# Kernel optimization log

Hardware: AMD Instinct MI355X
Metric: run time of the kernel (lower is better)

## Reference

```python
import jax, jax.numpy as jnp
import numpy as np

B, S, E, H = 4, 2048, 1024, 128  # batch, seq_len, n_embeddings, head_size


def setup_inputs() -> dict:
    key = jax.random.key(0)
    kx, kq, kk, kv = jax.random.split(key, 4)
    x = jax.random.normal(kx, (B, S, E), dtype=jnp.float32)
    # nn.Linear(E, H, bias=False) weights, stored transposed so proj = x @ W
    Wq = jax.random.normal(kq, (E, H), dtype=jnp.float32) * 0.02
    Wk = jax.random.normal(kk, (E, H), dtype=jnp.float32) * 0.02
    Wv = jax.random.normal(kv, (E, H), dtype=jnp.float32) * 0.02
    return {"x": x, "Wq": Wq, "Wk": Wk, "Wv": Wv}


def reference(x, Wq, Wk, Wv):
    # Single causal self-attention head (dropout = identity, eval mode).
    q = jnp.einsum("bse,eh->bsh", x, Wq)  # [B,S,H]
    k = jnp.einsum("bse,eh->bsh", x, Wk)
    v = jnp.einsum("bse,eh->bsh", x, Wv)
    scale = 1.0 / jnp.sqrt(jnp.asarray(H, dtype=x.dtype))
    scores = jnp.einsum("bqh,bkh->bqk", q, k) * scale  # [B,S,S]
    causal = jnp.tril(jnp.ones((S, S), dtype=bool))
    scores = jnp.where(causal, scores, jnp.asarray(-jnp.inf, dtype=scores.dtype))
    weights = jax.nn.softmax(scores, axis=-1)
    out = jnp.einsum("bqk,bkh->bqh", weights, v)  # [B,S,H]
    return out
```

## Files before the change

### kernel.cpp

```cpp
#include <hip/hip_runtime.h>
#include <math.h>

#define BB 4
#define SS 2048
#define EE 1024
#define HH 128
#define PLANE (BB * SS * HH)
#define BPLANE (SS * HH)
#define AUNITS 144

typedef __bf16 bf16x8 __attribute__((ext_vector_type(8)));
typedef __bf16 bf16x4 __attribute__((ext_vector_type(4)));
typedef float f32x4 __attribute__((ext_vector_type(4)));

#define QSCALE (0.08838834764831845f * 1.4426950408889634f)

__global__ __launch_bounds__(256) void prep_w(
    const float* __restrict__ Wq, const float* __restrict__ Wk,
    const float* __restrict__ Wv, __bf16* __restrict__ WT) {
  __shared__ float LT[32 * 33];
  const int p = blockIdx.x >> 7;
  const int r = blockIdx.x & 127;
  const int kb = (r >> 2) * 32, nb = (r & 3) * 32;
  const float* __restrict__ W = (p == 0) ? Wq : (p == 1) ? Wk : Wv;
  const int t = threadIdx.x;
  const int kr = t >> 3, nc4 = (t & 7) * 4;
  const float4 v = *(const float4*)&W[(size_t)(kb + kr) * HH + nb + nc4];
  LT[(nc4 + 0) * 33 + kr] = v.x;
  LT[(nc4 + 1) * 33 + kr] = v.y;
  LT[(nc4 + 2) * 33 + kr] = v.z;
  LT[(nc4 + 3) * 33 + kr] = v.w;
  __syncthreads();
  const int n = t >> 3, kc = (t & 7) * 4;
  bf16x4 o;
#pragma unroll
  for (int i = 0; i < 4; ++i) o[i] = (__bf16)LT[n * 33 + kc + i];
  *(bf16x4*)&WT[(size_t)p * (HH * EE) + (size_t)(nb + n) * EE + kb + kc] = o;
}

__global__ __launch_bounds__(512, 2) void qkv_proj(
    const float* __restrict__ x, const __bf16* __restrict__ WT,
    __bf16* __restrict__ qkv) {
  __shared__ __align__(16) char smem[81920];
  __bf16* xs = (__bf16*)smem;
  __bf16* wsd = (__bf16*)(smem + 40960);

  const int t = threadIdx.x, w = t >> 6, lane = t & 63;
  const int quad = lane >> 4, l16 = lane & 15;
  const int kg = w >> 2, wl = w & 3;
  const int t2 = t & 255;
  const int mb = blockIdx.x * 128;
  const int proj = blockIdx.y;
  const __bf16* __restrict__ WTp = WT + (size_t)proj * (HH * EE);
  const int wm = (wl >> 1) * 64, wn = (wl & 1) * 64;
  const int kb0 = kg * 512;

  f32x4 acc[4][4];
#pragma unroll
  for (int i = 0; i < 4; ++i)
#pragma unroll
    for (int j = 0; j < 4; ++j) acc[i][j] = (f32x4){0.f, 0.f, 0.f, 0.f};

  {
    __bf16* xb = xs + (size_t)(kg * 2) * 5120;
    __bf16* wb = wsd + (size_t)(kg * 2) * 5120;
#pragma unroll
    for (int i = 0; i < 4; ++i) {
      const int idx = t2 + i * 256;
      const int row = idx >> 3, kc = (idx & 7) * 4;
      const float4 v = *(const float4*)&x[(size_t)(mb + row) * EE + kb0 + kc];
      bf16x4 bv;
      bv[0] = (__bf16)v.x; bv[1] = (__bf16)v.y;
      bv[2] = (__bf16)v.z; bv[3] = (__bf16)v.w;
      *(bf16x4*)&xb[row * 40 + kc] = bv;
    }
#pragma unroll
    for (int i = 0; i < 2; ++i) {
      const int idx = t2 + i * 256;
      const int n = idx >> 2, kc8 = (idx & 3) * 8;
      *(bf16x8*)&wb[n * 40 + kc8] =
          *(const bf16x8*)&WTp[(size_t)n * EE + kb0 + kc8];
    }
  }
  __syncthreads();

  for (int kt = 0; kt < 16; ++kt) {
    const int cur = kt & 1;
    float4 xr[4];
    bf16x8 wr[2];
    if (kt < 15) {
      const int kb = kb0 + (kt + 1) * 32;
#pragma unroll
      for (int i = 0; i < 4; ++i) {
        const int idx = t2 + i * 256;
        const int row = idx >> 3, kc = (idx & 7) * 4;
        xr[i] = *(const float4*)&x[(size_t)(mb + row) * EE + kb + kc];
      }
#pragma unroll
      for (int i = 0; i < 2; ++i) {
        const int idx = t2 + i * 256;
        const int n = idx >> 2, kc8 = (idx & 3) * 8;
        wr[i] = *(const bf16x8*)&WTp[(size_t)n * EE + kb + kc8];
      }
    }

    const __bf16* xb = xs + (size_t)(kg * 2 + cur) * 5120;
    const __bf16* wb = wsd + (size_t)(kg * 2 + cur) * 5120;
    bf16x8 af[4], bfr[4];
#pragma unroll
    for (int i = 0; i < 4; ++i)
      af[i] = *(const bf16x8*)&xb[(wm + i * 16 + l16) * 40 + quad * 8];
#pragma unroll
    for (int j = 0; j < 4; ++j)
      bfr[j] = *(const bf16x8*)&wb[(wn + j * 16 + l16) * 40 + quad * 8];
#pragma unroll
    for (int i = 0; i < 4; ++i)
#pragma unroll
      for (int j = 0; j < 4; ++j)
        acc[i][j] = __builtin_amdgcn_mfma_f32_16x16x32_bf16(
            af[i], bfr[j], acc[i][j], 0, 0, 0);

    if (kt < 15) {
      __bf16* xb1 = xs + (size_t)(kg * 2 + (cur ^ 1)) * 5120;
      __bf16* wb1 = wsd + (size_t)(kg * 2 + (cur ^ 1)) * 5120;
#pragma unroll
      for (int i = 0; i < 4; ++i) {
        const int idx = t2 + i * 256;
        const int row = idx >> 3, kc = (idx & 7) * 4;
        bf16x4 bv;
        bv[0] = (__bf16)xr[i].x; bv[1] = (__bf16)xr[i].y;
        bv[2] = (__bf16)xr[i].z; bv[3] = (__bf16)xr[i].w;
        *(bf16x4*)&xb1[row * 40 + kc] = bv;
      }
#pragma unroll
      for (int i = 0; i < 2; ++i) {
        const int idx = t2 + i * 256;
        const int n = idx >> 2, kc8 = (idx & 3) * 8;
        *(bf16x8*)&wb1[n * 40 + kc8] = wr[i];
      }
    }
    __syncthreads();
  }

  float* mbuf = (float*)smem;
  if (kg == 1) {
    float* mb = mbuf + (size_t)wl * 4096;
#pragma unroll
    for (int i = 0; i < 4; ++i)
#pragma unroll
      for (int j = 0; j < 4; ++j)
#pragma unroll
        for (int rr = 0; rr < 4; ++rr)
          mb[(i * 16 + quad * 4 + rr) * 64 + j * 16 + l16] = acc[i][j][rr];
  }
  __syncthreads();
  if (kg == 0) {
    const float* mb = mbuf + (size_t)wl * 4096;
#pragma unroll
    for (int i = 0; i < 4; ++i)
#pragma unroll
      for (int j = 0; j < 4; ++j)
#pragma unroll
        for (int rr = 0; rr < 4; ++rr)
          acc[i][j][rr] += mb[(i * 16 + quad * 4 + rr) * 64 + j * 16 + l16];

    if (proj < 2) {
      const float scale = (proj == 0) ? QSCALE : 1.0f;
      __bf16* outp = qkv + (size_t)proj * PLANE;
#pragma unroll
      for (int i = 0; i < 4; ++i) {
        const int s0 = mb == 0 ? 0 : 0;
        const int srow = (blockIdx.x * 128) + wm + i * 16 + quad * 4;
#pragma unroll
        for (int j = 0; j < 4; ++j)
#pragma unroll
          for (int rr = 0; rr < 4; ++rr)
            outp[(size_t)(srow + rr) * HH + wn + j * 16 + l16] =
                (__bf16)(acc[i][j][rr] * scale);
      }
    } else {
      __bf16* vtp = qkv + 2 * (size_t)PLANE;
#pragma unroll
      for (int i = 0; i < 4; ++i) {
        const int srow = (blockIdx.x * 128) + wm + i * 16 + quad * 4;
        const int bb = srow >> 11, sl = srow & 2047;
#pragma unroll
        for (int j = 0; j < 4; ++j) {
          const int d = wn + j * 16 + l16;
          bf16x4 vv;
#pragma unroll
          for (int rr = 0; rr < 4; ++rr) vv[rr] = (__bf16)acc[i][j][rr];
          *(bf16x4*)&vtp[(size_t)bb * BPLANE + (size_t)d * SS + sl] = vv;
        }
      }
    }
  }
}

__global__ __launch_bounds__(256, 2) void flash_attn_mfma(
    const __bf16* __restrict__ qkv, float* __restrict__ out,
    __bf16* __restrict__ Opart, float* __restrict__ lpart) {
  __shared__ __align__(16) __bf16 K_s[2][64 * 136];
  __shared__ __align__(16) __bf16 VT_s[2][128 * 72];

  const int t = threadIdx.x, w = t >> 6, lane = t & 63;
  const int quad = lane >> 4, l16 = lane & 15;
  const int b = blockIdx.x & 3;
  const int r = (AUNITS - 1) - (blockIdx.x >> 2);
  int g = 0;
  while (2 * (g + 1) * (g + 2) <= r) ++g;
  const int rem = r - 2 * g * (g + 1);
  const int nc = g + 1;
  const int tloc = rem / nc, c = rem % nc;
  const int tile = 4 * g + tloc;
  const int qrb = tile * 64;
  const int k0 = c * 256;
  const int kend = min(k0 + 256, qrb + 64);
  const int ntiles = (kend - k0) >> 6;
  const int qsb = qrb + w * 16;

  const size_t bq = (size_t)b * BPLANE;
  const __bf16* __restrict__ qp = qkv + bq;
  const __bf16* __restrict__ kp = qkv + PLANE + bq;
  const __bf16* __restrict__ vt = qkv + 2 * (size_t)PLANE + bq;

  bf16x8 qf[4];
#pragma unroll
  for (int cc = 0; cc < 4; ++cc)
    qf[cc] = *(const bf16x8*)&qp[(size_t)(qsb + l16) * HH + cc * 32 + quad * 8];

  f32x4 of[8];
#pragma unroll
  for (int f = 0; f < 8; ++f) of[f] = (f32x4){0.f, 0.f, 0.f, 0.f};
  float lp = 0.f;

  {
#pragma unroll
    for (int i = 0; i < 4; ++i) {
      const int idx = t + i * 256;
      const int row = idx >> 4, dc = (idx & 15) * 8;
      const int lam = (row & 32) + ((row & 4) ? 16 : 0) +
                      (((row & 31) >> 3) << 2) + (row & 3);
      *(bf16x8*)&K_s[0][lam * 136 + dc] =
          *(const bf16x8*)&kp[(size_t)(k0 + row) * HH + dc];
    }
#pragma unroll
    for (int i = 0; i < 4; ++i) {
      const int idx = t + i * 256;
      const int d = idx >> 3, kc = (idx & 7) * 8;
      *(bf16x8*)&VT_s[0][d * 72 + kc] =
          *(const bf16x8*)&vt[(size_t)d * SS + k0 + kc];
    }
  }
  __syncthreads();

  for (int jt = 0; jt < ntiles; ++jt) {
    const int cur = jt & 1;
    bf16x8 krg[4], vrg[4];
    if (jt + 1 < ntiles) {
      const int kb2 = k0 + (jt + 1) * 64;
#pragma unroll
      for (int i = 0; i < 4; ++i) {
        const int idx = t + i * 256;
        const int row = idx >> 4, dc = (idx & 15) * 8;
        krg[i] = *(const bf16x8*)&kp[(size_t)(kb2 + row) * HH + dc];
      }
#pragma unroll
      for (int i = 0; i < 4; ++i) {
        const int idx = t + i * 256;
        const int d = idx >> 3, kc = (idx & 7) * 8;
        vrg[i] = *(const bf16x8*)&vt[(size_t)d * SS + kb2 + kc];
      }
    }

    const __bf16* Kc = K_s[cur];
    const __bf16* Vc = VT_s[cur];
#pragma unroll
    for (int s32 = 0; s32 < 2; ++s32) {
      const int kabs = k0 + jt * 64 + s32 * 32;
      if (kabs <= qsb + 15) {
        bf16x8 ku[4], kv[4];
#pragma unroll
        for (int cc = 0; cc < 4; ++cc) {
          ku[cc] = *(const bf16x8*)&Kc[(s32 * 32 + l16) * 136 + cc * 32 + quad * 8];
          kv[cc] = *(const bf16x8*)&Kc[(s32 * 32 + 16 + l16) * 136 + cc * 32 + quad * 8];
        }
        f32x4 su = (f32x4){0.f, 0.f, 0.f, 0.f};
        f32x4 sv = (f32x4){0.f, 0.f, 0.f, 0.f};
#pragma unroll
        for (int cc = 0; cc < 4; ++cc) {
          su = __builtin_amdgcn_mfma_f32_16x16x32_bf16(ku[cc], qf[cc], su, 0, 0, 0);
          sv = __builtin_amdgcn_mfma_f32_16x16x32_bf16(kv[cc], qf[cc], sv, 0, 0, 0);
        }
        const int qg = qsb + l16;
        bf16x8 pa;
#pragma unroll
        for (int rr = 0; rr < 4; ++rr) {
          const int kU = kabs + quad * 8 + rr;
          const float eU = (kU <= qg) ? exp2f(su[rr]) : 0.f;
          const float eV = (kU + 4 <= qg) ? exp2f(sv[rr]) : 0.f;
          pa[rr] = (__bf16)eU;
          pa[4 + rr] = (__bf16)eV;
          lp += eU + eV;
        }
#pragma unroll
        for (int f = 0; f < 8; ++f) {
          const bf16x8 vb =
              *(const bf16x8*)&Vc[(f * 16 + l16) * 72 + s32 * 32 + quad * 8];
          of[f] = __builtin_amdgcn_mfma_f32_16x16x32_bf16(pa, vb, of[f], 0, 0, 0);
        }
      }
    }

    if (jt + 1 < ntiles) {
      const int nxt = cur ^ 1;
#pragma unroll
      for (int i = 0; i < 4; ++i) {
        const int idx = t + i * 256;
        const int row = idx >> 4, dc = (idx & 15) * 8;
        const int lam = (row & 32) + ((row & 4) ? 16 : 0) +
                        (((row & 31) >> 3) << 2) + (row & 3);
        *(bf16x8*)&K_s[nxt][lam * 136 + dc] = krg[i];
      }
#pragma unroll
      for (int i = 0; i < 4; ++i) {
        const int idx = t + i * 256;
        const int d = idx >> 3, kc = (idx & 7) * 8;
        *(bf16x8*)&VT_s[nxt][d * 72 + kc] = vrg[i];
      }
    }
    __syncthreads();
  }

  lp += __shfl_xor(lp, 16);
  lp += __shfl_xor(lp, 32);

  if (nc == 1) {
#pragma unroll
    for (int rr = 0; rr < 4; ++rr) {
      const float lrow = __shfl(lp, quad * 4 + rr);
      const float inv = 1.0f / lrow;
#pragma unroll
      for (int f = 0; f < 8; ++f)
        out[bq + (size_t)(qsb + quad * 4 + rr) * HH + f * 16 + l16] =
            of[f][rr] * inv;
    }
  } else {
    const int u = b * AUNITS + r;
    __bf16* op = Opart + (size_t)u * 8192;
#pragma unroll
    for (int f = 0; f < 8; ++f)
#pragma unroll
      for (int rr = 0; rr < 4; ++rr)
        op[(w * 16 + quad * 4 + rr) * 128 + f * 16 + l16] = (__bf16)of[f][rr];
    if (quad == 0) lpart[u * 64 + w * 16 + l16] = lp;
  }
}

__global__ __launch_bounds__(256) void attn_merge(
    const __bf16* __restrict__ Opart, const float* __restrict__ lpart,
    float* __restrict__ out) {
  const int b = blockIdx.x / 28;
  const int tile = 4 + (blockIdx.x % 28);
  const int g = tile >> 2, nc = g + 1, tloc = tile - 4 * g;
  const int u0 = b * AUNITS + 2 * g * (g + 1) + tloc * nc;
  const int t = threadIdx.x;
#pragma unroll
  for (int i = 0; i < 4; ++i) {
    const int idx = t + i * 256;
    const int e0 = idx * 8;
    const int row = e0 >> 7;
    float acc[8] = {0.f, 0.f, 0.f, 0.f, 0.f, 0.f, 0.f, 0.f};
    float lsum = 0.f;
    for (int cc = 0; cc < nc; ++cc) {
      const bf16x8 pv = *(const bf16x8*)&Opart[(size_t)(u0 + cc) * 8192 + e0];
#pragma unroll
      for (int k = 0; k < 8; ++k) acc[k] += (float)pv[k];
      lsum += lpart[(u0 + cc) * 64 + row];
    }
    const float inv = 1.0f / lsum;
    float4 r0, r1;
    r0.x = acc[0] * inv; r0.y = acc[1] * inv; r0.z = acc[2] * inv; r0.w = acc[3] * inv;
    r1.x = acc[4] * inv; r1.y = acc[5] * inv; r1.z = acc[6] * inv; r1.w = acc[7] * inv;
    float* op = out + (size_t)b * BPLANE + (size_t)tile * 8192 + e0;
    ((float4*)op)[0] = r0;
    ((float4*)op)[1] = r1;
  }
}

extern "C" void kernel_launch(void* const* d_in, const int* in_sizes, int n_in,
                              void* d_out, int out_size, void* d_ws, size_t ws_size,
                              hipStream_t stream) {
  const float* x  = (const float*)d_in[0];
  const float* Wq = (const float*)d_in[1];
  const float* Wk = (const float*)d_in[2];
  const float* Wv = (const float*)d_in[3];
  float* out = (float*)d_out;

  char* wsb = (char*)d_ws;
  __bf16* qkv = (__bf16*)wsb;
  __bf16* WT = (__bf16*)(wsb + (size_t)3 * PLANE * 2);
  __bf16* Opart = (__bf16*)(wsb + (size_t)3 * PLANE * 2 + (size_t)3 * HH * EE * 2);
  float* lpart = (float*)(wsb + (size_t)3 * PLANE * 2 + (size_t)3 * HH * EE * 2 +
                          (size_t)BB * AUNITS * 8192 * 2);

  prep_w<<<384, 256, 0, stream>>>(Wq, Wk, Wv, WT);
  qkv_proj<<<dim3(64, 3), 512, 0, stream>>>(x, WT, qkv);
  flash_attn_mfma<<<BB * AUNITS, 256, 0, stream>>>(qkv, out, Opart, lpart);
  attn_merge<<<BB * 28, 256, 0, stream>>>(Opart, lpart, out);
}
```

Baseline: 129.6 us.

## Shrink projection tiles, split attention into finer KV chunks, single-buffer LDS

The QKV projection moves from 128-row, split-K 512-thread blocks to 32-row 256-thread blocks with no split-K reduction, launching many more blocks. Attention work units are re-partitioned into 128-key chunks (272 units per batch instead of 144) with a new triangular index mapping, and the merge kernel is adjusted to match. The flash kernel drops LDS double buffering in favour of register prefetch plus two barriers per tile, cutting shared memory so three blocks fit per CU. The aim is better load balance and occupancy across CUs. The cost is more partial outputs to merge, more barriers, and more reloading of the projection weight tiles.

```diff
diff --git a/kernel.cpp b/kernel.cpp
--- a/kernel.cpp
+++ b/kernel.cpp
@@ -7,7 +7,7 @@
 #define HH 128
 #define PLANE (BB * SS * HH)
 #define BPLANE (SS * HH)
-#define AUNITS 144
+#define AUNITS 272
 
 typedef __bf16 bf16x8 __attribute__((ext_vector_type(8)));
 typedef __bf16 bf16x4 __attribute__((ext_vector_type(4)));
@@ -38,184 +38,130 @@
   *(bf16x4*)&WT[(size_t)p * (HH * EE) + (size_t)(nb + n) * EE + kb + kc] = o;
 }
 
-__global__ __launch_bounds__(512, 2) void qkv_proj(
+__global__ __launch_bounds__(256, 4) void qkv_proj(
     const float* __restrict__ x, const __bf16* __restrict__ WT,
     __bf16* __restrict__ qkv) {
-  __shared__ __align__(16) char smem[81920];
-  __bf16* xs = (__bf16*)smem;
-  __bf16* wsd = (__bf16*)(smem + 40960);
+  __shared__ __align__(16) __bf16 xs[32 * 72];
+  __shared__ __align__(16) __bf16 wsd[128 * 72];
 
   const int t = threadIdx.x, w = t >> 6, lane = t & 63;
   const int quad = lane >> 4, l16 = lane & 15;
-  const int kg = w >> 2, wl = w & 3;
-  const int t2 = t & 255;
-  const int mb = blockIdx.x * 128;
+  const int mb = blockIdx.x * 32;
   const int proj = blockIdx.y;
   const __bf16* __restrict__ WTp = WT + (size_t)proj * (HH * EE);
-  const int wm = (wl >> 1) * 64, wn = (wl & 1) * 64;
-  const int kb0 = kg * 512;
-
-  f32x4 acc[4][4];
+
+  const int xrow0 = t >> 4, xkc0 = (t & 15) * 4;
+  const int wn0 = t >> 3, wkc0 = (t & 7) * 8;
+
+  f32x4 acc[2][2];
+#pragma unroll
+  for (int i = 0; i < 2; ++i)
+#pragma unroll
+    for (int j = 0; j < 2; ++j) acc[i][j] = (f32x4){0.f, 0.f, 0.f, 0.f};
+
+  float4 xr[2];
+  bf16x8 wr[4];
+#pragma unroll
+  for (int i = 0; i < 2; ++i)
+    xr[i] = *(const float4*)&x[(size_t)(mb + xrow0 + i * 16) * EE + xkc0];
 #pragma unroll
   for (int i = 0; i < 4; ++i)
-#pragma unroll
-    for (int j = 0; j < 4; ++j) acc[i][j] = (f32x4){0.f, 0.f, 0.f, 0.f};
-
-  {
-    __bf16* xb = xs + (size_t)(kg * 2) * 5120;
-    __bf16* wb = wsd + (size_t)(kg * 2) * 5120;
-#pragma unroll
-    for (int i = 0; i < 4; ++i) {
-      const int idx = t2 + i * 256;
-      const int row = idx >> 3, kc = (idx & 7) * 4;
-      const float4 v = *(const float4*)&x[(size_t)(mb + row) * EE + kb0 + kc];
+    wr[i] = *(const bf16x8*)&WTp[(size_t)(wn0 + i * 32) * EE + wkc0];
+
+  for (int kt = 0; kt < 16; ++kt) {
+    __syncthreads();
+#pragma unroll
+    for (int i = 0; i < 2; ++i) {
       bf16x4 bv;
-      bv[0] = (__bf16)v.x; bv[1] = (__bf16)v.y;
-      bv[2] = (__bf16)v.z; bv[3] = (__bf16)v.w;
-      *(bf16x4*)&xb[row * 40 + kc] = bv;
-    }
-#pragma unroll
-    for (int i = 0; i < 2; ++i) {
-      const int idx = t2 + i * 256;
-      const int n = idx >> 2, kc8 = (idx & 3) * 8;
-      *(bf16x8*)&wb[n * 40 + kc8] =
-          *(const bf16x8*)&WTp[(size_t)n * EE + kb0 + kc8];
-    }
-  }
-  __syncthreads();
-
-  for (int kt = 0; kt < 16; ++kt) {
-    const int cur = kt & 1;
-    float4 xr[4];
-    bf16x8 wr[2];
+      bv[0] = (__bf16)xr[i].x; bv[1] = (__bf16)xr[i].y;
+      bv[2] = (__bf16)xr[i].z; bv[3] = (__bf16)xr[i].w;
+      *(bf16x4*)&xs[(xrow0 + i * 16) * 72 + xkc0] = bv;
+    }
+#pragma unroll
+    for (int i = 0; i < 4; ++i)
+      *(bf16x8*)&wsd[(wn0 + i * 32) * 72 + wkc0] = wr[i];
+    __syncthreads();
+
     if (kt < 15) {
-      const int kb = kb0 + (kt + 1) * 32;
-#pragma unroll
-      for (int i = 0; i < 4; ++i) {
-        const int idx = t2 + i * 256;
-        const int row = idx >> 3, kc = (idx & 7) * 4;
-        xr[i] = *(const float4*)&x[(size_t)(mb + row) * EE + kb + kc];
-      }
-#pragma unroll
-      for (int i = 0; i < 2; ++i) {
-        const int idx = t2 + i * 256;
-        const int n = idx >> 2, kc8 = (idx & 3) * 8;
-        wr[i] = *(const bf16x8*)&WTp[(size_t)n * EE + kb + kc8];
-      }
-    }
-
-    const __bf16* xb = xs + (size_t)(kg * 2 + cur) * 5120;
-    const __bf16* wb = wsd + (size_t)(kg * 2 + cur) * 5120;
-    bf16x8 af[4], bfr[4];
-#pragma unroll
-    for (int i = 0; i < 4; ++i)
-      af[i] = *(const bf16x8*)&xb[(wm + i * 16 + l16) * 40 + quad * 8];
-#pragma unroll
-    for (int j = 0; j < 4; ++j)
-      bfr[j] = *(const bf16x8*)&wb[(wn + j * 16 + l16) * 40 + quad * 8];
-#pragma unroll
-    for (int i = 0; i < 4; ++i)
-#pragma unroll
-      for (int j = 0; j < 4; ++j)
-        acc[i][j] = __builtin_amdgcn_mfma_f32_16x16x32_bf16(
-            af[i], bfr[j], acc[i][j], 0, 0, 0);
-
-    if (kt < 15) {
-      __bf16* xb1 = xs + (size_t)(kg * 2 + (cur ^ 1)) * 5120;
-      __bf16* wb1 = wsd + (size_t)(kg * 2 + (cur ^ 1)) * 5120;
-#pragma unroll
-      for (int i = 0; i < 4; ++i) {
-        const int idx = t2 + i * 256;
-        const int row = idx >> 3, kc = (idx & 7) * 4;
-        bf16x4 bv;
-        bv[0] = (__bf16)xr[i].x; bv[1] = (__bf16)xr[i].y;
-        bv[2] = (__bf16)xr[i].z; bv[3] = (__bf16)xr[i].w;
-        *(bf16x4*)&xb1[row * 40 + kc] = bv;
-      }
-#pragma unroll
-      for (int i = 0; i < 2; ++i) {
-        const int idx = t2 + i * 256;
-        const int n = idx >> 2, kc8 = (idx & 3) * 8;
-        *(bf16x8*)&wb1[n * 40 + kc8] = wr[i];
-      }
-    }
-    __syncthreads();
-  }
-
-  float* mbuf = (float*)smem;
-  if (kg == 1) {
-    float* mb = mbuf + (size_t)wl * 4096;
-#pragma unroll
-    for (int i = 0; i < 4; ++i)
-#pragma unroll
-      for (int j = 0; j < 4; ++j)
+      const int kb = (kt + 1) * 64;
+#pragma unroll
+      for (int i = 0; i < 2; ++i)
+        xr[i] = *(const float4*)&x[(size_t)(mb + xrow0 + i * 16) * EE + kb + xkc0];
+#pragma unroll
+      for (int i = 0; i < 4; ++i)
+        wr[i] = *(const bf16x8*)&WTp[(size_t)(wn0 + i * 32) * EE + kb + wkc0];
+    }
+
+    bf16x8 af[2][2], bfr[2][2];
+#pragma unroll
+    for (int mi = 0; mi < 2; ++mi)
+#pragma unroll
+      for (int kc = 0; kc < 2; ++kc)
+        af[mi][kc] = *(const bf16x8*)&xs[(mi * 16 + l16) * 72 + kc * 32 + quad * 8];
+#pragma unroll
+    for (int ni = 0; ni < 2; ++ni)
+#pragma unroll
+      for (int kc = 0; kc < 2; ++kc)
+        bfr[ni][kc] =
+            *(const bf16x8*)&wsd[(w * 32 + ni * 16 + l16) * 72 + kc * 32 + quad * 8];
+#pragma unroll
+    for (int kc = 0; kc < 2; ++kc)
+#pragma unroll
+      for (int mi = 0; mi < 2; ++mi)
+#pragma unroll
+        for (int ni = 0; ni < 2; ++ni)
+          acc[mi][ni] = __builtin_amdgcn_mfma_f32_16x16x32_bf16(
+              af[mi][kc], bfr[ni][kc], acc[mi][ni], 0, 0, 0);
+  }
+
+  if (proj < 2) {
+    const float scale = (proj == 0) ? QSCALE : 1.0f;
+    __bf16* outp = qkv + (size_t)proj * PLANE;
+#pragma unroll
+    for (int mi = 0; mi < 2; ++mi) {
+      const int srow = mb + mi * 16 + quad * 4;
+#pragma unroll
+      for (int ni = 0; ni < 2; ++ni) {
+        const int col = w * 32 + ni * 16 + l16;
 #pragma unroll
         for (int rr = 0; rr < 4; ++rr)
-          mb[(i * 16 + quad * 4 + rr) * 64 + j * 16 + l16] = acc[i][j][rr];
-  }
-  __syncthreads();
-  if (kg == 0) {
-    const float* mb = mbuf + (size_t)wl * 4096;
-#pragma unroll
-    for (int i = 0; i < 4; ++i)
-#pragma unroll
-      for (int j = 0; j < 4; ++j)
-#pragma unroll
-        for (int rr = 0; rr < 4; ++rr)
-          acc[i][j][rr] += mb[(i * 16 + quad * 4 + rr) * 64 + j * 16 + l16];
-
-    if (proj < 2) {
-      const float scale = (proj == 0) ? QSCALE : 1.0f;
-      __bf16* outp = qkv + (size_t)proj * PLANE;
-#pragma unroll
-      for (int i = 0; i < 4; ++i) {
-        const int s0 = mb == 0 ? 0 : 0;
-        const int srow = (blockIdx.x * 128) + wm + i * 16 + quad * 4;
-#pragma unroll
-        for (int j = 0; j < 4; ++j)
-#pragma unroll
-          for (int rr = 0; rr < 4; ++rr)
-            outp[(size_t)(srow + rr) * HH + wn + j * 16 + l16] =
-                (__bf16)(acc[i][j][rr] * scale);
-      }
-    } else {
-      __bf16* vtp = qkv + 2 * (size_t)PLANE;
-#pragma unroll
-      for (int i = 0; i < 4; ++i) {
-        const int srow = (blockIdx.x * 128) + wm + i * 16 + quad * 4;
-        const int bb = srow >> 11, sl = srow & 2047;
-#pragma unroll
-        for (int j = 0; j < 4; ++j) {
-          const int d = wn + j * 16 + l16;
-          bf16x4 vv;
-#pragma unroll
-          for (int rr = 0; rr < 4; ++rr) vv[rr] = (__bf16)acc[i][j][rr];
-          *(bf16x4*)&vtp[(size_t)bb * BPLANE + (size_t)d * SS + sl] = vv;
-        }
-      }
-    }
-  }
-}
-
-__global__ __launch_bounds__(256, 2) void flash_attn_mfma(
+          outp[(size_t)(srow + rr) * HH + col] = (__bf16)(acc[mi][ni][rr] * scale);
+      }
+    }
+  } else {
+    __bf16* vtp = qkv + 2 * (size_t)PLANE;
+#pragma unroll
+    for (int mi = 0; mi < 2; ++mi) {
+      const int srow = mb + mi * 16 + quad * 4;
+      const int bb = srow >> 11, sl = srow & 2047;
+#pragma unroll
+      for (int ni = 0; ni < 2; ++ni) {
+        const int d = w * 32 + ni * 16 + l16;
+        bf16x4 vv;
+#pragma unroll
+        for (int rr = 0; rr < 4; ++rr) vv[rr] = (__bf16)acc[mi][ni][rr];
+        *(bf16x4*)&vtp[(size_t)bb * BPLANE + (size_t)d * SS + sl] = vv;
+      }
+    }
+  }
+}
+
+__global__ __launch_bounds__(256, 3) void flash_attn_mfma(
     const __bf16* __restrict__ qkv, float* __restrict__ out,
     __bf16* __restrict__ Opart, float* __restrict__ lpart) {
-  __shared__ __align__(16) __bf16 K_s[2][64 * 136];
-  __shared__ __align__(16) __bf16 VT_s[2][128 * 72];
+  __shared__ __align__(16) __bf16 K_s[64 * 136];
+  __shared__ __align__(16) __bf16 VT_s[128 * 72];
 
   const int t = threadIdx.x, w = t >> 6, lane = t & 63;
   const int quad = lane >> 4, l16 = lane & 15;
   const int b = blockIdx.x & 3;
   const int r = (AUNITS - 1) - (blockIdx.x >> 2);
-  int g = 0;
-  while (2 * (g + 1) * (g + 2) <= r) ++g;
-  const int rem = r - 2 * g * (g + 1);
-  const int nc = g + 1;
-  const int tloc = rem / nc, c = rem % nc;
-  const int tile = 4 * g + tloc;
-  const int qrb = tile * 64;
-  const int k0 = c * 256;
-  const int kend = min(k0 + 256, qrb + 64);
+  int tt = 0;
+  while ((((tt + 2) * (tt + 2)) >> 2) <= r) ++tt;
+  const int c = r - (((tt + 1) * (tt + 1)) >> 2);
+  const int qrb = tt * 64;
+  const int k0 = c * 128;
+  const int kend = min(k0 + 128, qrb + 64);
   const int ntiles = (kend - k0) >> 6;
   const int qsb = qrb + w * 16;
 
@@ -234,29 +180,39 @@
   for (int f = 0; f < 8; ++f) of[f] = (f32x4){0.f, 0.f, 0.f, 0.f};
   float lp = 0.f;
 
-  {
+  const int krow = t >> 2, kdc = (t & 3) * 8;
+  bf16x8 krg[4], vrg[4];
+#pragma unroll
+  for (int i = 0; i < 4; ++i) {
+    const int idx = t + i * 256;
+    const int row = idx >> 4, dc = (idx & 15) * 8;
+    krg[i] = *(const bf16x8*)&kp[(size_t)(k0 + row) * HH + dc];
+  }
+#pragma unroll
+  for (int i = 0; i < 4; ++i) {
+    const int idx = t + i * 256;
+    const int d = idx >> 3, kc = (idx & 7) * 8;
+    vrg[i] = *(const bf16x8*)&vt[(size_t)d * SS + k0 + kc];
+  }
+
+  for (int jt = 0; jt < ntiles; ++jt) {
+    __syncthreads();
 #pragma unroll
     for (int i = 0; i < 4; ++i) {
       const int idx = t + i * 256;
       const int row = idx >> 4, dc = (idx & 15) * 8;
       const int lam = (row & 32) + ((row & 4) ? 16 : 0) +
                       (((row & 31) >> 3) << 2) + (row & 3);
-      *(bf16x8*)&K_s[0][lam * 136 + dc] =
-          *(const bf16x8*)&kp[(size_t)(k0 + row) * HH + dc];
+      *(bf16x8*)&K_s[lam * 136 + dc] = krg[i];
     }
 #pragma unroll
     for (int i = 0; i < 4; ++i) {
       const int idx = t + i * 256;
       const int d = idx >> 3, kc = (idx & 7) * 8;
-      *(bf16x8*)&VT_s[0][d * 72 + kc] =
-          *(const bf16x8*)&vt[(size_t)d * SS + k0 + kc];
-    }
-  }
-  __syncthreads();
-
-  for (int jt = 0; jt < ntiles; ++jt) {
-    const int cur = jt & 1;
-    bf16x8 krg[4], vrg[4];
+      *(bf16x8*)&VT_s[d * 72 + kc] = vrg[i];
+    }
+    __syncthreads();
+
     if (jt + 1 < ntiles) {
       const int kb2 = k0 + (jt + 1) * 64;
 #pragma unroll
@@ -273,8 +229,6 @@
       }
     }
 
-    const __bf16* Kc = K_s[cur];
-    const __bf16* Vc = VT_s[cur];
 #pragma unroll
     for (int s32 = 0; s32 < 2; ++s32) {
       const int kabs = k0 + jt * 64 + s32 * 32;
@@ -282,8 +236,8 @@
         bf16x8 ku[4], kv[4];
 #pragma unroll
         for (int cc = 0; cc < 4; ++cc) {
-          ku[cc] = *(const bf16x8*)&Kc[(s32 * 32 + l16) * 136 + cc * 32 + quad * 8];
-          kv[cc] = *(const bf16x8*)&Kc[(s32 * 32 + 16 + l16) * 136 + cc * 32 + quad * 8];
+          ku[cc] = *(const bf16x8*)&K_s[(s32 * 32 + l16) * 136 + cc * 32 + quad * 8];
+          kv[cc] = *(const bf16x8*)&K_s[(s32 * 32 + 16 + l16) * 136 + cc * 32 + quad * 8];
         }
         f32x4 su = (f32x4){0.f, 0.f, 0.f, 0.f};
         f32x4 sv = (f32x4){0.f, 0.f, 0.f, 0.f};
@@ -306,36 +260,17 @@
 #pragma unroll
         for (int f = 0; f < 8; ++f) {
           const bf16x8 vb =
-              *(const bf16x8*)&Vc[(f * 16 + l16) * 72 + s32 * 32 + quad * 8];
+              *(const bf16x8*)&VT_s[(f * 16 + l16) * 72 + s32 * 32 + quad * 8];
           of[f] = __builtin_amdgcn_mfma_f32_16x16x32_bf16(pa, vb, of[f], 0, 0, 0);
         }
       }
     }
-
-    if (jt + 1 < ntiles) {
-      const int nxt = cur ^ 1;
-#pragma unroll
-      for (int i = 0; i < 4; ++i) {
-        const int idx = t + i * 256;
-        const int row = idx >> 4, dc = (idx & 15) * 8;
-        const int lam = (row & 32) + ((row & 4) ? 16 : 0) +
-                        (((row & 31) >> 3) << 2) + (row & 3);
-        *(bf16x8*)&K_s[nxt][lam * 136 + dc] = krg[i];
-      }
-#pragma unroll
-      for (int i = 0; i < 4; ++i) {
-        const int idx = t + i * 256;
-        const int d = idx >> 3, kc = (idx & 7) * 8;
-        *(bf16x8*)&VT_s[nxt][d * 72 + kc] = vrg[i];
-      }
-    }
-    __syncthreads();
   }
 
   lp += __shfl_xor(lp, 16);
   lp += __shfl_xor(lp, 32);
 
-  if (nc == 1) {
+  if (tt < 2) {
 #pragma unroll
     for (int rr = 0; rr < 4; ++rr) {
       const float lrow = __shfl(lp, quad * 4 + rr);
@@ -360,16 +295,16 @@
 __global__ __launch_bounds__(256) void attn_merge(
     const __bf16* __restrict__ Opart, const float* __restrict__ lpart,
     float* __restrict__ out) {
-  const int b = blockIdx.x / 28;
-  const int tile = 4 + (blockIdx.x % 28);
-  const int g = tile >> 2, nc = g + 1, tloc = tile - 4 * g;
-  const int u0 = b * AUNITS + 2 * g * (g + 1) + tloc * nc;
+  const int b = blockIdx.x / 30;
+  const int tile = 2 + (blockIdx.x % 30);
+  const int nc = (tile + 2) >> 1;
+  const int u0 = b * AUNITS + (((tile + 1) * (tile + 1)) >> 2);
   const int t = threadIdx.x;
 #pragma unroll
   for (int i = 0; i < 4; ++i) {
     const int idx = t + i * 256;
     const int e0 = idx * 8;
-    const int row = e0 >> 7;
+    const int row = idx >> 4;
     float acc[8] = {0.f, 0.f, 0.f, 0.f, 0.f, 0.f, 0.f, 0.f};
     float lsum = 0.f;
     for (int cc = 0; cc < nc; ++cc) {
@@ -405,7 +340,7 @@
                           (size_t)BB * AUNITS * 8192 * 2);
 
   prep_w<<<384, 256, 0, stream>>>(Wq, Wk, Wv, WT);
-  qkv_proj<<<dim3(64, 3), 512, 0, stream>>>(x, WT, qkv);
+  qkv_proj<<<dim3(BB * SS / 32, 3), 256, 0, stream>>>(x, WT, qkv);
   flash_attn_mfma<<<BB * AUNITS, 256, 0, stream>>>(qkv, out, Opart, lpart);
-  attn_merge<<<BB * 28, 256, 0, stream>>>(Opart, lpart, out);
-}
+  attn_merge<<<BB * 30, 256, 0, stream>>>(Opart, lpart, out);
+}
```

After: 129.0 us. No clear change (-0.4%).
